# Kernel tuning notes

Measured on AMD Instinct MI355X. Metric: run time of the kernel, lower is better.

Reference implementation:

```python
import jax, jax.numpy as jnp
import numpy as np

KERNEL = (7, 7)
NUM_CH = 4
EPS = 1e-06
ROPE_BASE = 10000.0


def _rel_dist():
    coords = [np.arange(k, dtype=np.float32) - k // 2 for k in KERNEL]
    g = np.meshgrid(*coords, indexing='ij')
    d = np.sqrt(sum(gi ** 2 for gi in g))
    return jnp.asarray(d.reshape(-1)), float(d.max())


def silu(x):
    return x * jax.nn.sigmoid(x)


def rmsnorm(x, w):
    rms = jnp.sqrt(jnp.mean(x * x, axis=-1, keepdims=True) + EPS)
    return x / rms * w


def apply_rope(x):
    # x: (B, L, H, D); positions run over dim -2 (matches torch default)
    H, D = x.shape[-2], x.shape[-1]
    half = D // 2
    pos = jnp.arange(H, dtype=jnp.float32)
    freqs = 1.0 / (ROPE_BASE ** (jnp.arange(half, dtype=x.dtype) / half))
    ang = pos[:, None] * freqs  # (H, half)
    cos, sin = jnp.cos(ang), jnp.sin(ang)
    x1, x2 = x[..., :half], x[..., half:2 * half]
    return jnp.concatenate([x1 * cos - x2 * sin, x1 * sin + x2 * cos], axis=-1)


def unfold2d(x):
    # x: (B, Hs, Ws, C) -> (B, Hs, Ws, k1*k2, C), row-major kernel order
    B, Hs, Ws, C = x.shape
    k1, k2 = KERNEL
    xp = jnp.pad(x, ((0, 0), ((k1 - 1) // 2, k1 // 2), ((k2 - 1) // 2, k2 // 2), (0, 0)))
    wins = [xp[:, i:i + Hs, j:j + Ws, :] for i in range(k1) for j in range(k2)]
    return jnp.stack(wins, axis=3)


def setup_inputs() -> dict:
    key = jax.random.key(0)
    ks = jax.random.split(key, 8)
    C = 256
    x = jax.random.normal(ks[0], (2, 64, 64, C), dtype=jnp.float32)
    W_qkv = jax.random.normal(ks[1], (C, 3 * C), dtype=jnp.float32) * 0.02
    w_qnorm = jnp.ones((C // NUM_CH,), dtype=jnp.float32)
    w_knorm = jnp.ones((C // NUM_CH,), dtype=jnp.float32)
    W_wp = jax.random.normal(ks[2], (C, 2 * NUM_CH), dtype=jnp.float32) * 0.02
    b_wp = jax.random.normal(ks[3], (2 * NUM_CH,), dtype=jnp.float32) * 0.02
    w_onorm = jnp.ones((C,), dtype=jnp.float32)
    W_out = jax.random.normal(ks[4], (C, C), dtype=jnp.float32) * 0.02
    W_gate = jax.random.normal(ks[5], (C, C), dtype=jnp.float32) * 0.02
    b_gate = 2.0 * jnp.ones((C,), dtype=jnp.float32)
    return {"x": x, "W_qkv": W_qkv, "w_qnorm": w_qnorm, "w_knorm": w_knorm,
            "W_wp": W_wp, "b_wp": b_wp, "w_onorm": w_onorm, "W_out": W_out,
            "W_gate": W_gate, "b_gate": b_gate}


def reference(x, W_qkv, w_qnorm, w_knorm, W_wp, b_wp, w_onorm, W_out, W_gate, b_gate):
    rel_dist, max_dist = _rel_dist()
    B, Hs, Ws, C = x.shape
    L = Hs * Ws
    H = NUM_CH
    D = C // H
    Wsz = KERNEL[0] * KERNEL[1]
    scale = D ** (-0.5)

    qkv = silu(x @ W_qkv)
    q, k, v = jnp.split(qkv, 3, axis=-1)

    q_flat = apply_rope(rmsnorm(q.reshape(B, L, H, D), w_qnorm))
    k_flat = apply_rope(rmsnorm(k.reshape(B, L, H, D), w_knorm))
    k = k_flat.reshape(B, Hs, Ws, C)

    wp = silu(x @ W_wp + b_wp)  # (B, Hs, Ws, 2H)
    width_raw, sharp_raw = jnp.split(wp, 2, axis=-1)
    width = jax.nn.sigmoid(width_raw) * max_dist + 0.5
    sharpness = jax.nn.sigmoid(sharp_raw) * 9.5 + 0.5

    k_win = unfold2d(k).reshape(B, L, Wsz, H, D)
    v_win = unfold2d(v).reshape(B, L, Wsz, H, D)

    scores = jnp.einsum('blhd,blwhd->blhw', q_flat, k_win) * scale
    width_f = width.reshape(B, L, H, 1)
    sharp_f = sharpness.reshape(B, L, H, 1)
    soft_mask = jax.nn.sigmoid((width_f - rel_dist) * sharp_f)
    scores = scores - (1.0 - soft_mask) * 10000.0
    attn = jax.nn.softmax(scores, axis=-1)

    out = jnp.einsum('blhw,blwhd->blhd', attn, v_win).reshape(B, Hs, Ws, C)
    out = rmsnorm(out, w_onorm)

    gate = jax.nn.sigmoid(silu(v @ W_gate + b_gate))
    merged = gate * v + (1.0 - gate) * out
    return silu(merged @ W_out)
```

## Files before the change

kernel.cpp:

```cpp
#include <hip/hip_runtime.h>
#include <hip/hip_fp16.h>
#include <math.h>

__device__ __forceinline__ float sigm(float x)  { return 1.0f / (1.0f + __expf(-x)); }
__device__ __forceinline__ float siluf(float x) { return x * sigm(x); }

typedef _Float16 half8  __attribute__((ext_vector_type(8)));
typedef _Float16 half4  __attribute__((ext_vector_type(4)));
typedef float    f32x4  __attribute__((ext_vector_type(4)));

__device__ __forceinline__ void gld16(const void* g, void* l) {
    __builtin_amdgcn_global_load_lds(
        (const __attribute__((address_space(1))) unsigned*)g,
        (__attribute__((address_space(3))) unsigned*)l, 16, 0, 0);
}

template <int MI, int AMODE>
__device__ __forceinline__ void gemm_core16(
    const __half* __restrict__ A16,
    const __half* __restrict__ Bhi, const __half* __restrict__ Blo,
    int nbs, int m0, int n0, int t, f32x4 (&acc)[MI][4])
{
    __shared__ short As[MI * 1024], BsHi[4096], BsLo[4096];
    const int lane = t & 63, wave = t >> 6;
    const int wm = (wave >> 1) * (MI << 4), wn = (wave & 1) << 6;
    const int fr = lane & 15, fq = lane >> 4;

    for (int kb = 0; kb < 8; ++kb) {
        __syncthreads();
#pragma unroll
        for (int hf = 0; hf < MI / 2; ++hf) {
            const int rr = wave * (MI << 3) + (hf << 4);
            size_t ga;
            if (AMODE == 0)
                ga = (((size_t)(kb * 8192 + m0 + rr)) << 5) + (lane << 3);
            else
                ga = (((size_t)(m0 + rr + (lane >> 2))) << 8) + (kb << 5) + ((lane & 3) << 3);
            gld16(A16 + ga, &As[rr << 5]);
        }
#pragma unroll
        for (int hf = 0; hf < 2; ++hf) {
            const int rr = (wave << 5) + (hf << 4);
            const size_t gb = (((size_t)(kb * nbs + n0 + rr)) << 5) + (lane << 3);
            gld16(Bhi + gb, &BsHi[rr << 5]);
            gld16(Blo + gb, &BsLo[rr << 5]);
        }
        __syncthreads();

        half8 a[MI], bh[4], bl[4];
#pragma unroll
        for (int i = 0; i < MI; ++i)
            a[i] = *(const half8*)&As[((wm + (i << 4) + fr) << 5) + (fq << 3)];
#pragma unroll
        for (int i = 0; i < 4; ++i) {
            const int boff = ((wn + (i << 4) + fr) << 5) + (fq << 3);
            bh[i] = *(const half8*)&BsHi[boff];
            bl[i] = *(const half8*)&BsLo[boff];
        }
#pragma unroll
        for (int mi = 0; mi < MI; ++mi)
#pragma unroll
            for (int ni = 0; ni < 4; ++ni) {
                acc[mi][ni] = __builtin_amdgcn_mfma_f32_16x16x32_f16(a[mi], bh[ni], acc[mi][ni], 0, 0, 0);
                acc[mi][ni] = __builtin_amdgcn_mfma_f32_16x16x32_f16(a[mi], bl[ni], acc[mi][ni], 0, 0, 0);
            }
    }
}

__global__ __launch_bounds__(256) void prep_kernel(
    const float* __restrict__ x, const float* __restrict__ Wqkv,
    const float* __restrict__ Wgate, const float* __restrict__ Wout,
    const float* __restrict__ Wwp, const float* __restrict__ bwp,
    __half* __restrict__ xh,
    __half* __restrict__ wqh, __half* __restrict__ wql,
    __half* __restrict__ wgh, __half* __restrict__ wgl,
    __half* __restrict__ woh, __half* __restrict__ wol,
    float* __restrict__ width, float* __restrict__ sharp)
{
    __shared__ float xs[32][260];
    const int t = threadIdx.x;
    const int blk = blockIdx.x;
    if (blk < 256) {
        const int row0 = blk << 5;
        for (int e = t; e < 2048; e += 256) {
            int r = e >> 6, cc = (e & 63) << 2;
            *(float4*)&xs[r][cc] = *(const float4*)&x[(size_t)(row0 + r) * 256 + cc];
        }
        __syncthreads();
        const int r = t >> 3, kb = t & 7;
        __half hibuf[32];
#pragma unroll
        for (int i = 0; i < 32; ++i)
            hibuf[i] = __float2half(xs[r][(kb << 5) + i]);
        const size_t ob = ((size_t)(kb * 8192 + row0 + r)) << 5;
#pragma unroll
        for (int i = 0; i < 4; ++i)
            *(int4*)&xh[ob + (i << 3)] = *(int4*)&hibuf[i << 3];
        float acc = 0.f;
#pragma unroll 8
        for (int k = 0; k < 256; ++k) acc += xs[r][k] * Wwp[k * 8 + kb];
        float s = sigm(siluf(acc + bwp[kb]));
        const int row = row0 + r;
        if (kb < 4) width[row * 4 + kb] = s * 4.242640687119285f + 0.5f;
        else        sharp[row * 4 + kb - 4] = s * 9.5f + 0.5f;
    } else {
        const float* W; __half *Whi, *Wlo; int N, nb0, ncnt;
        if (blk < 288)      { W = Wqkv;  Whi = wqh; Wlo = wql; N = 768; nb0 = (blk - 256) * 24; ncnt = 24; }
        else if (blk < 296) { W = Wgate; Whi = wgh; Wlo = wgl; N = 256; nb0 = (blk - 288) * 32; ncnt = 32; }
        else                { W = Wout;  Whi = woh; Wlo = wol; N = 256; nb0 = (blk - 296) * 32; ncnt = 32; }
        for (int j = 0; j < ncnt; ++j)
            xs[j][t] = W[(size_t)t * N + nb0 + j];
        __syncthreads();
        for (int c = t; c < ncnt * 8; c += 256) {
            const int j = c >> 3, kb = c & 7;
            __half hibuf[32], lobuf[32];
#pragma unroll
            for (int i = 0; i < 32; ++i) {
                float v = xs[j][(kb << 5) + i];
                __half hv = __float2half(v);
                hibuf[i] = hv;
                lobuf[i] = __float2half(v - __half2float(hv));
            }
            const size_t ob = ((size_t)(kb * N + nb0 + j)) << 5;
#pragma unroll
            for (int i = 0; i < 4; ++i) {
                *(int4*)&Whi[ob + (i << 3)] = *(int4*)&hibuf[i << 3];
                *(int4*)&Wlo[ob + (i << 3)] = *(int4*)&lobuf[i << 3];
            }
        }
    }
}

__global__ __launch_bounds__(256, 3) void gemm_qkv(
    const __half* __restrict__ xh,
    const __half* __restrict__ wqh, const __half* __restrict__ wql,
    const float* __restrict__ wq, const float* __restrict__ wk,
    __half* __restrict__ qh, __half* __restrict__ kh, __half* __restrict__ vh)
{
    const int t  = threadIdx.x;
    const int m0 = blockIdx.y << 7, n0 = blockIdx.x << 7;
    f32x4 acc[4][4] = {};
    gemm_core16<4, 0>(xh, wqh, wql, 768, m0, n0, t, acc);

    const int lane = t & 63, wave = t >> 6;
    const int wm = (wave >> 1) << 6, wn = (wave & 1) << 6;
    const int fr = lane & 15, fq = lane >> 4;
    const int gc0 = n0 + wn;
    const int seg = gc0 >> 8;
    const int h   = (gc0 >> 6) & 3;
    const int hc0 = h << 6;

#pragma unroll
    for (int mi = 0; mi < 4; ++mi)
#pragma unroll
        for (int ni = 0; ni < 4; ++ni)
#pragma unroll
            for (int r = 0; r < 4; ++r)
                acc[mi][ni][r] = siluf(acc[mi][ni][r]);

    if (seg == 2) {
#pragma unroll
        for (int mi = 0; mi < 4; ++mi)
#pragma unroll
            for (int r = 0; r < 4; ++r) {
                const size_t row = m0 + wm + (mi << 4) + (fq << 2) + r;
#pragma unroll
                for (int ni = 0; ni < 4; ++ni)
                    vh[row * 256 + hc0 + (ni << 4) + fr] = __float2half(acc[mi][ni][r]);
            }
    } else {
        const float* wnorm = seg ? wk : wq;
        float wv[4];
#pragma unroll
        for (int ni = 0; ni < 4; ++ni) wv[ni] = wnorm[(ni << 4) + fr];
        float cs[2], sn[2];
#pragma unroll
        for (int j = 0; j < 2; ++j) {
            const int d = (j << 4) + fr;
            const float freq = powf(10000.f, -(float)d * (1.f / 32.f));
            const float ang = (float)h * freq;
            cs[j] = cosf(ang); sn[j] = sinf(ang);
        }
        __half* dstbase = (seg ? kh : qh);
#pragma unroll
        for (int mi = 0; mi < 4; ++mi)
#pragma unroll
            for (int r = 0; r < 4; ++r) {
                float ss = acc[mi][0][r] * acc[mi][0][r] + acc[mi][1][r] * acc[mi][1][r]
                         + acc[mi][2][r] * acc[mi][2][r] + acc[mi][3][r] * acc[mi][3][r];
                ss += __shfl_xor(ss, 1); ss += __shfl_xor(ss, 2);
                ss += __shfl_xor(ss, 4); ss += __shfl_xor(ss, 8);
                const float rinv = 1.f / sqrtf(ss * (1.f / 64.f) + 1e-6f);
                float xv[4];
#pragma unroll
                for (int ni = 0; ni < 4; ++ni) xv[ni] = acc[mi][ni][r] * rinv * wv[ni];
                const float o0 = xv[0] * cs[0] - xv[2] * sn[0];
                const float o2 = xv[0] * sn[0] + xv[2] * cs[0];
                const float o1 = xv[1] * cs[1] - xv[3] * sn[1];
                const float o3 = xv[1] * sn[1] + xv[3] * cs[1];
                const size_t row = m0 + wm + (mi << 4) + (fq << 2) + r;
                __half* dst = dstbase + row * 256 + hc0;
                dst[fr]      = __float2half(o0);
                dst[16 + fr] = __float2half(o1);
                dst[32 + fr] = __float2half(o2);
                dst[48 + fr] = __float2half(o3);
            }
    }
}

__global__ __launch_bounds__(256, 3) void gemm_gate(
    const __half* __restrict__ vh,
    const __half* __restrict__ wgh, const __half* __restrict__ wgl,
    const float* __restrict__ bias, const float* __restrict__ attn_o,
    const float* __restrict__ sumsq4, const float* __restrict__ w_onorm,
    __half* __restrict__ mh)
{
    const int t  = threadIdx.x;
    const int m0 = blockIdx.y << 6, n0 = blockIdx.x << 7;
    f32x4 acc[2][4] = {};
    gemm_core16<2, 1>(vh, wgh, wgl, 256, m0, n0, t, acc);

    const int lane = t & 63, wave = t >> 6;
    const int wm = (wave >> 1) << 5, wn = (wave & 1) << 6;
    const int fr = lane & 15, fq = lane >> 4;

    float rmsf[2][4];
#pragma unroll
    for (int mi = 0; mi < 2; ++mi)
#pragma unroll
        for (int r = 0; r < 4; ++r) {
            const int m = m0 + wm + (mi << 4) + (fq << 2) + r;
            float4 s4 = *(const float4*)&sumsq4[(size_t)m * 4];
            rmsf[mi][r] = 1.f / sqrtf((s4.x + s4.y + s4.z + s4.w) * (1.f / 256.f) + 1e-6f);
        }

#pragma unroll
    for (int mi = 0; mi < 2; ++mi)
#pragma unroll
        for (int ni = 0; ni < 4; ++ni) {
            const int n  = n0 + wn + (ni << 4) + fr;
            const int mb = m0 + wm + (mi << 4) + (fq << 2);
            const float bb  = bias[n];
            const float won = w_onorm[n];
#pragma unroll
            for (int r = 0; r < 4; ++r) {
                const int m = mb + r;
                const float g  = sigm(siluf(acc[mi][ni][r] + bb));
                const float vv = __half2float(vh[(size_t)m * 256 + n]);
                const float oo = attn_o[(size_t)m * 256 + n] * rmsf[mi][r] * won;
                mh[(size_t)m * 256 + n] = __float2half(g * vv + (1.f - g) * oo);
            }
        }
}

__global__ __launch_bounds__(256, 3) void gemm_out(
    const __half* __restrict__ mh,
    const __half* __restrict__ woh, const __half* __restrict__ wol,
    float* __restrict__ out)
{
    const int t  = threadIdx.x;
    const int m0 = blockIdx.y << 6, n0 = blockIdx.x << 7;
    f32x4 acc[2][4] = {};
    gemm_core16<2, 1>(mh, woh, wol, 256, m0, n0, t, acc);

    const int lane = t & 63, wave = t >> 6;
    const int wm = (wave >> 1) << 5, wn = (wave & 1) << 6;
    const int fr = lane & 15, fq = lane >> 4;
#pragma unroll
    for (int mi = 0; mi < 2; ++mi)
#pragma unroll
        for (int ni = 0; ni < 4; ++ni) {
            const int n  = n0 + wn + (ni << 4) + fr;
            const int mb = m0 + wm + (mi << 4) + (fq << 2);
#pragma unroll
            for (int r = 0; r < 4; ++r)
                out[(size_t)(mb + r) * 256 + n] = siluf(acc[mi][ni][r]);
        }
}

#define PT 216

__global__ __launch_bounds__(256, 2) void attn_mfma(
    const __half* __restrict__ qh, const __half* __restrict__ kh,
    const __half* __restrict__ vh, const float* __restrict__ width,
    const float* __restrict__ sharp, float* __restrict__ attn_o,
    float* __restrict__ sumsq4)
{
    __shared__ short smem[27648];
    short* Ksh = smem;
    short* Psh = smem;
    short* Vt  = smem + 13824;

    const int t = threadIdx.x;
    const int lane = t & 63, wave = t >> 6;
    const int fr = lane & 15, fq = lane >> 4;
    const int patch = blockIdx.x, h = blockIdx.y, b = blockIdx.z;
    const int pr0 = (patch >> 3) << 3, pc0 = (patch & 7) << 3;

    float wd[4], sh[4]; int lq[4];
#pragma unroll
    for (int r = 0; r < 4; ++r) {
        const int q = (wave << 4) + (fq << 2) + r;
        lq[r] = (pr0 + (q >> 3)) * 64 + pc0 + (q & 7);
        wd[r] = width[((b << 12) + lq[r]) * 4 + h];
        sh[r] = sharp[((b << 12) + lq[r]) * 4 + h];
    }

    const int qrow = (wave << 4) + fr;
    const int lqr = (pr0 + (qrow >> 3)) * 64 + pc0 + (qrow & 7);
    const __half* qptr = qh + (((size_t)(b << 12) + lqr) << 8) + (h << 6) + (fq << 3);
    half8 a0 = *(const half8*)qptr;
    half8 a1 = *(const half8*)(qptr + 32);

    const int srow = t >> 5;
    const int d2 = (t & 31) << 1;
    const size_t cbase = (((size_t)b << 12) * 256) + (size_t)h * 64 + d2;

    unsigned kb[25], vb[25];
#pragma unroll
    for (int p5 = 0; p5 < 25; ++p5) {
        const int prow = p5 * 8 + srow;
        const int pi = prow / 14, pj = prow - pi * 14;
        const int gr = pr0 - 3 + pi, gc = pc0 - 3 + pj;
        const bool ok = (prow < 196) & ((unsigned)gr < 64u) & ((unsigned)gc < 64u);
        const int grc = min(max(gr, 0), 63), gcc = min(max(gc, 0), 63);
        const size_t off = cbase + (size_t)(grc * 64 + gcc) * 256;
        unsigned kv = *(const unsigned*)(kh + off);
        unsigned vv = *(const unsigned*)(vh + off);
        kb[p5] = ok ? kv : 0u;
        vb[p5] = ok ? vv : 0u;
    }

    const int chunk = d2 >> 3, dlo = d2 & 7;
#pragma unroll
    for (int p5 = 0; p5 < 25; ++p5) {
        const int prow = p5 * 8 + srow;
        *(unsigned*)&Ksh[(prow << 6) + ((chunk ^ (prow & 7)) << 3) + dlo] = kb[p5];
        Vt[(d2)     * PT + prow] = (short)(vb[p5] & 0xffffu);
        Vt[(d2 + 1) * PT + prow] = (short)(vb[p5] >> 16);
    }
    if (t < 128) {
        const int rr = 200 + (t >> 4);
        *(unsigned*)&Ksh[(rr << 6) + (((t & 15) ^ ((rr & 7) << 1)) << 2)] = 0u;
    }
    for (int i = t; i < 64 * 20; i += 256)
        Vt[(i / 20) * PT + 196 + (i % 20)] = 0;
    __syncthreads();

    f32x4 sc[13];
#pragma unroll
    for (int tl = 0; tl < 13; ++tl) {
        const int kr = (tl << 4) + fr;
        half8 b0 = *(const half8*)&Ksh[(kr << 6) + (((0 + fq) ^ (kr & 7)) << 3)];
        half8 b1 = *(const half8*)&Ksh[(kr << 6) + (((4 + fq) ^ (kr & 7)) << 3)];
        f32x4 z = {0.f, 0.f, 0.f, 0.f};
        z = __builtin_amdgcn_mfma_f32_16x16x32_f16(a0, b0, z, 0, 0, 0);
        sc[tl] = __builtin_amdgcn_mfma_f32_16x16x32_f16(a1, b1, z, 0, 0, 0);
    }

    float mx[4] = {-3e38f, -3e38f, -3e38f, -3e38f};
#pragma unroll
    for (int tl = 0; tl < 13; ++tl) {
        const int p = (tl << 4) + fr;
        const int pi = p / 14, pj = p - pi * 14;
        const bool pvld = p < 196;
#pragma unroll
        for (int r = 0; r < 4; ++r) {
            const int q = (wave << 4) + (fq << 2) + r;
            const int di = pi - 3 - ((q >> 3) & 7), dj = pj - 3 - (q & 7);
            const bool win = pvld & ((unsigned)(di + 3) <= 6u) & ((unsigned)(dj + 3) <= 6u);
            const float rel = sqrtf((float)(di * di + dj * dj));
            const float mk = sigm((wd[r] - rel) * sh[r]);
            float s = sc[tl][r] * 0.125f - (1.f - mk) * 10000.f;
            s = win ? s : -3e38f;
            sc[tl][r] = s;
            mx[r] = fmaxf(mx[r], s);
        }
    }
#pragma unroll
    for (int r = 0; r < 4; ++r) {
        mx[r] = fmaxf(mx[r], __shfl_xor(mx[r], 1));
        mx[r] = fmaxf(mx[r], __shfl_xor(mx[r], 2));
        mx[r] = fmaxf(mx[r], __shfl_xor(mx[r], 4));
        mx[r] = fmaxf(mx[r], __shfl_xor(mx[r], 8));
    }
    float sm[4] = {0.f, 0.f, 0.f, 0.f};
#pragma unroll
    for (int tl = 0; tl < 13; ++tl)
#pragma unroll
        for (int r = 0; r < 4; ++r) {
            const float e = __expf(sc[tl][r] - mx[r]);
            sc[tl][r] = e; sm[r] += e;
        }
#pragma unroll
    for (int r = 0; r < 4; ++r) {
        sm[r] += __shfl_xor(sm[r], 1);
        sm[r] += __shfl_xor(sm[r], 2);
        sm[r] += __shfl_xor(sm[r], 4);
        sm[r] += __shfl_xor(sm[r], 8);
        sm[r] = 1.f / sm[r];
    }

    __syncthreads();
#pragma unroll
    for (int tl = 0; tl < 13; ++tl)
#pragma unroll
        for (int r = 0; r < 4; ++r) {
            __half pv = __float2half(sc[tl][r] * sm[r]);
            Psh[((wave << 4) + (fq << 2) + r) * PT + (tl << 4) + fr] = *(short*)&pv;
        }
    __syncthreads();

    f32x4 o[4] = {};
    const int pra = (wave << 4) + fr;
#pragma unroll
    for (int s = 0; s < 6; ++s) {
        half8 pa = *(const half8*)&Psh[pra * PT + (fq << 3) + (s << 5)];
#pragma unroll
        for (int dt = 0; dt < 4; ++dt) {
            half8 vbf = *(const half8*)&Vt[((dt << 4) + fr) * PT + (fq << 3) + (s << 5)];
            o[dt] = __builtin_amdgcn_mfma_f32_16x16x32_f16(pa, vbf, o[dt], 0, 0, 0);
        }
    }
    {
        half4 pa = *(const half4*)&Psh[pra * PT + 192 + (fq << 2)];
#pragma unroll
        for (int dt = 0; dt < 4; ++dt) {
            half4 vbf = *(const half4*)&Vt[((dt << 4) + fr) * PT + 192 + (fq << 2)];
            o[dt] = __builtin_amdgcn_mfma_f32_16x16x16f16(pa, vbf, o[dt], 0, 0, 0);
        }
    }

#pragma unroll
    for (int r = 0; r < 4; ++r) {
        float ss = o[0][r]*o[0][r] + o[1][r]*o[1][r] + o[2][r]*o[2][r] + o[3][r]*o[3][r];
        ss += __shfl_xor(ss, 1); ss += __shfl_xor(ss, 2);
        ss += __shfl_xor(ss, 4); ss += __shfl_xor(ss, 8);
        const size_t rowb = (((size_t)(b << 12) + lq[r]) << 8) + h * 64;
#pragma unroll
        for (int dt = 0; dt < 4; ++dt)
            attn_o[rowb + (dt << 4) + fr] = o[dt][r];
        if (fr == 0) sumsq4[(((b << 12) + lq[r]) << 2) + h] = ss;
    }
}

extern "C" void kernel_launch(void* const* d_in, const int* in_sizes, int n_in,
                              void* d_out, int out_size, void* d_ws, size_t ws_size,
                              hipStream_t stream)
{
    const float* x      = (const float*)d_in[0];
    const float* W_qkv  = (const float*)d_in[1];
    const float* w_qn   = (const float*)d_in[2];
    const float* w_kn   = (const float*)d_in[3];
    const float* W_wp   = (const float*)d_in[4];
    const float* b_wp   = (const float*)d_in[5];
    const float* w_on   = (const float*)d_in[6];
    const float* W_out  = (const float*)d_in[7];
    const float* W_gate = (const float*)d_in[8];
    const float* b_gate = (const float*)d_in[9];
    float* out = (float*)d_out;

    __half* ws16 = (__half*)d_ws;
    __half* xh  = ws16;
    __half* wqh = xh  + 2097152;
    __half* wql = wqh + 196608;
    __half* wgh = wql + 196608;
    __half* wgl = wgh + 65536;
    __half* woh = wgl + 65536;
    __half* wol = woh + 65536;
    __half* qhp = wol + 65536;
    __half* khp = qhp + 2097152;
    __half* vhp = khp + 2097152;
    __half* mh  = vhp + 2097152;
    float* attn_o = (float*)(mh + 2097152);
    float* widthp = attn_o + 2097152;
    float* sharpp = widthp + 32768;
    float* sumsq4 = sharpp + 32768;

    prep_kernel<<<304, 256, 0, stream>>>(x, W_qkv, W_gate, W_out, W_wp, b_wp,
                                         xh, wqh, wql, wgh, wgl, woh, wol,
                                         widthp, sharpp);
    gemm_qkv<<<dim3(6, 64), 256, 0, stream>>>(xh, wqh, wql, w_qn, w_kn,
                                              qhp, khp, vhp);
    attn_mfma<<<dim3(64, 4, 2), 256, 0, stream>>>(qhp, khp, vhp, widthp, sharpp,
                                                  attn_o, sumsq4);
    gemm_gate<<<dim3(2, 128), 256, 0, stream>>>(vhp, wgh, wgl, b_gate,
                                                attn_o, sumsq4, w_on, mh);
    gemm_out<<<dim3(2, 128), 256, 0, stream>>>(mh, woh, wol, out);
}
```

Measured before the change: 155.8 us.

## Stream K tiles directly into LDS and shrink LDS to raise attention occupancy

The attention kernel now loads the K neighbourhood tile with async global-to-LDS 16-byte loads instead of staging it through registers and writing it back with swizzled stores. Out-of-image K rows now hold clamped data, so their scores are zeroed in the mask step rather than by zero-filling K. V is gathered two positions per thread and packed into 32-bit transposed stores. The LDS row pitch shrinks from 216 to 208, the explicit padding zero-fill is dropped, and launch bounds move to 3 blocks per CU. The barrier before the P·V step becomes a wave-local LDS wait, which relies on each wave reading only the P rows it wrote itself. The direct-to-LDS loads depend on the barrier also waiting for outstanding vector-memory loads.

```diff
diff --git a/kernel.cpp b/kernel.cpp
--- a/kernel.cpp
+++ b/kernel.cpp
@@ -278,24 +278,25 @@
         }
 }
 
-#define PT 216
-
-__global__ __launch_bounds__(256, 2) void attn_mfma(
+#define PT 208
+
+__global__ __launch_bounds__(256, 3) void attn_mfma(
     const __half* __restrict__ qh, const __half* __restrict__ kh,
     const __half* __restrict__ vh, const float* __restrict__ width,
     const float* __restrict__ sharp, float* __restrict__ attn_o,
     float* __restrict__ sumsq4)
 {
-    __shared__ short smem[27648];
+    __shared__ short smem[26624];
     short* Ksh = smem;
     short* Psh = smem;
-    short* Vt  = smem + 13824;
+    short* Vt  = smem + 13312;
 
     const int t = threadIdx.x;
     const int lane = t & 63, wave = t >> 6;
     const int fr = lane & 15, fq = lane >> 4;
     const int patch = blockIdx.x, h = blockIdx.y, b = blockIdx.z;
     const int pr0 = (patch >> 3) << 3, pc0 = (patch & 7) << 3;
+    const size_t cbase = (((size_t)b << 20)) + ((size_t)h << 6);
 
     float wd[4], sh[4]; int lq[4];
 #pragma unroll
@@ -306,6 +307,23 @@
         sh[r] = sharp[((b << 12) + lq[r]) * 4 + h];
     }
 
+    {
+        const int lr = lane >> 3;
+        const int doff = (((lane & 7) ^ (lr & 7)) << 3);
+#pragma unroll
+        for (int ci = 0; ci < 7; ++ci) {
+            const int c = wave + (ci << 2);
+            if (c < 26) {
+                const int pr = (c << 3) + lr;
+                const int pi = pr / 14, pj = pr - pi * 14;
+                const int grc = min(max(pr0 - 3 + pi, 0), 63);
+                const int gcc = min(max(pc0 - 3 + pj, 0), 63);
+                gld16(kh + cbase + (size_t)((grc << 6) + gcc) * 256 + doff,
+                      &Ksh[c << 9]);
+            }
+        }
+    }
+
     const int qrow = (wave << 4) + fr;
     const int lqr = (pr0 + (qrow >> 3)) * 64 + pc0 + (qrow & 7);
     const __half* qptr = qh + (((size_t)(b << 12) + lqr) << 8) + (h << 6) + (fq << 3);
@@ -314,37 +332,29 @@
 
     const int srow = t >> 5;
     const int d2 = (t & 31) << 1;
-    const size_t cbase = (((size_t)b << 12) * 256) + (size_t)h * 64 + d2;
-
-    unsigned kb[25], vb[25];
-#pragma unroll
-    for (int p5 = 0; p5 < 25; ++p5) {
-        const int prow = p5 * 8 + srow;
-        const int pi = prow / 14, pj = prow - pi * 14;
-        const int gr = pr0 - 3 + pi, gc = pc0 - 3 + pj;
-        const bool ok = (prow < 196) & ((unsigned)gr < 64u) & ((unsigned)gc < 64u);
-        const int grc = min(max(gr, 0), 63), gcc = min(max(gc, 0), 63);
-        const size_t off = cbase + (size_t)(grc * 64 + gcc) * 256;
-        unsigned kv = *(const unsigned*)(kh + off);
-        unsigned vv = *(const unsigned*)(vh + off);
-        kb[p5] = ok ? kv : 0u;
-        vb[p5] = ok ? vv : 0u;
-    }
-
-    const int chunk = d2 >> 3, dlo = d2 & 7;
-#pragma unroll
-    for (int p5 = 0; p5 < 25; ++p5) {
-        const int prow = p5 * 8 + srow;
-        *(unsigned*)&Ksh[(prow << 6) + ((chunk ^ (prow & 7)) << 3) + dlo] = kb[p5];
-        Vt[(d2)     * PT + prow] = (short)(vb[p5] & 0xffffu);
-        Vt[(d2 + 1) * PT + prow] = (short)(vb[p5] >> 16);
-    }
-    if (t < 128) {
-        const int rr = 200 + (t >> 4);
-        *(unsigned*)&Ksh[(rr << 6) + (((t & 15) ^ ((rr & 7) << 1)) << 2)] = 0u;
-    }
-    for (int i = t; i < 64 * 20; i += 256)
-        Vt[(i / 20) * PT + 196 + (i % 20)] = 0;
+    unsigned v0[13], v1[13];
+#pragma unroll
+    for (int j = 0; j < 13; ++j) {
+        const int p = (j << 4) + (srow << 1);
+#pragma unroll
+        for (int e = 0; e < 2; ++e) {
+            const int pp = p + e;
+            const int pi = pp / 14, pj = pp - pi * 14;
+            const int gr = pr0 - 3 + pi, gc = pc0 - 3 + pj;
+            const bool ok = (pp < 196) & ((unsigned)gr < 64u) & ((unsigned)gc < 64u);
+            const int grc = min(max(gr, 0), 63), gcc = min(max(gc, 0), 63);
+            const unsigned vv = *(const unsigned*)(vh + cbase + (size_t)((grc << 6) + gcc) * 256 + d2);
+            (e ? v1 : v0)[j] = ok ? vv : 0u;
+        }
+    }
+#pragma unroll
+    for (int j = 0; j < 13; ++j) {
+        const int p = (j << 4) + (srow << 1);
+        const unsigned lo = (v0[j] & 0xffffu) | (v1[j] << 16);
+        const unsigned hi = (v0[j] >> 16) | (v1[j] & 0xffff0000u);
+        *(unsigned*)&Vt[d2 * PT + p]       = lo;
+        *(unsigned*)&Vt[(d2 + 1) * PT + p] = hi;
+    }
     __syncthreads();
 
     f32x4 sc[13];
@@ -364,6 +374,7 @@
         const int p = (tl << 4) + fr;
         const int pi = p / 14, pj = p - pi * 14;
         const bool pvld = p < 196;
+        const bool inb = pvld & ((unsigned)(pr0 - 3 + pi) < 64u) & ((unsigned)(pc0 - 3 + pj) < 64u);
 #pragma unroll
         for (int r = 0; r < 4; ++r) {
             const int q = (wave << 4) + (fq << 2) + r;
@@ -371,7 +382,8 @@
             const bool win = pvld & ((unsigned)(di + 3) <= 6u) & ((unsigned)(dj + 3) <= 6u);
             const float rel = sqrtf((float)(di * di + dj * dj));
             const float mk = sigm((wd[r] - rel) * sh[r]);
-            float s = sc[tl][r] * 0.125f - (1.f - mk) * 10000.f;
+            const float s0 = inb ? sc[tl][r] * 0.125f : 0.f;
+            float s = s0 - (1.f - mk) * 10000.f;
             s = win ? s : -3e38f;
             sc[tl][r] = s;
             mx[r] = fmaxf(mx[r], s);
@@ -409,7 +421,7 @@
             __half pv = __float2half(sc[tl][r] * sm[r]);
             Psh[((wave << 4) + (fq << 2) + r) * PT + (tl << 4) + fr] = *(short*)&pv;
         }
-    __syncthreads();
+    asm volatile("s_waitcnt lgkmcnt(0)" ::: "memory");
 
     f32x4 o[4] = {};
     const int pra = (wave << 4) + fr;
```

New measurement: 156.6 us. No clear change (+0.5%).
